# Performance work log

Measured on AMD Instinct MI355X. Metric: run time of the kernel, lower is better.

## Reference

```python
import jax, jax.numpy as jnp
import numpy as np

N_NODES = 100000
N_EDGES = 1280000
D_IN = 64
D_HID = 64
D_OUT = 1
N_GRAPHS = 512


def setup_inputs() -> dict:
    key = jax.random.key(0)
    ks = jax.random.split(key, 12)
    x = jax.random.normal(ks[0], (N_NODES, D_IN), dtype=jnp.float32)
    edge_index = jax.random.randint(ks[1], (2, N_EDGES), 0, N_NODES, dtype=jnp.int32)
    batch = jnp.sort(jax.random.randint(ks[2], (N_NODES,), 0, N_GRAPHS, dtype=jnp.int32))
    s = 0.1
    w0 = jax.random.normal(ks[3], (D_IN, D_HID), dtype=jnp.float32) * s
    b0 = jnp.zeros((D_HID,), dtype=jnp.float32)
    w1 = jax.random.normal(ks[4], (D_HID, D_HID), dtype=jnp.float32) * s
    b1 = jnp.zeros((D_HID,), dtype=jnp.float32)
    w2 = jax.random.normal(ks[5], (D_HID, D_HID), dtype=jnp.float32) * s
    b2 = jnp.zeros((D_HID,), dtype=jnp.float32)
    fc_w = jax.random.normal(ks[6], (D_HID, D_OUT), dtype=jnp.float32) * s
    fc_b = jnp.zeros((D_OUT,), dtype=jnp.float32)
    return {"x": x, "edge_index": edge_index, "batch": batch,
            "w0": w0, "b0": b0, "w1": w1, "b1": b1, "w2": w2, "b2": b2,
            "fc_w": fc_w, "fc_b": fc_b}


def _gcn_conv(x, w, b, src, dst):
    # PyG GCNConv: h = x @ W; out_i = sum_j norm_ij * h_j over (A + I), sym norm.
    h = x @ w                                           # [N, H]
    ones = jnp.ones((src.shape[0],), dtype=h.dtype)
    deg = jax.ops.segment_sum(ones, dst, num_segments=N_NODES) + 1.0  # +1 self-loop
    dinv = jax.lax.rsqrt(deg)                           # [N]
    norm = dinv[src] * dinv[dst]                        # [E]
    agg = jax.ops.segment_sum(h[src] * norm[:, None], dst, num_segments=N_NODES)
    agg = agg + h * (dinv * dinv)[:, None]              # self-loop term
    return agg + b


def reference(x, edge_index, batch, w0, b0, w1, b1, w2, b2, fc_w, fc_b):
    src, dst = edge_index[0], edge_index[1]
    # 3 stacked GCNConv + relu (dropout is identity in eval mode)
    h = jax.nn.relu(_gcn_conv(x, w0, b0, src, dst))
    h = jax.nn.relu(_gcn_conv(h, w1, b1, src, dst))
    h = jax.nn.relu(_gcn_conv(h, w2, b2, src, dst))
    # global mean pool per graph
    sums = jax.ops.segment_sum(h, batch, num_segments=N_GRAPHS)        # [G, H]
    cnt = jax.ops.segment_sum(jnp.ones((N_NODES,), h.dtype), batch, num_segments=N_GRAPHS)
    mean = sums / jnp.maximum(cnt, 1.0)[:, None]
    return mean @ fc_w + fc_b                            # [G, 1]
```

## Files before the change

kernel.cpp:

```cpp
#include <hip/hip_runtime.h>
#include <hip/hip_fp16.h>
#include <type_traits>

#define N_NODES 100000
#define N_EDGES 1280000
#define N_GRAPHS 512
#define NBK 196
#define CHUNK 3200
#define NCH 400
#define CAP 8192
#define CAPH 4096
#define GEMM_BLOCKS 391

typedef _Float16 v8h __attribute__((ext_vector_type(8)));
typedef float v4f __attribute__((ext_vector_type(4)));

__device__ inline void fmix_lo(float& acc, unsigned h2, float n) {
    asm volatile("v_fma_mix_f32 %0, %1, %2, %0 op_sel:[0,0,0] op_sel_hi:[1,0,0]"
                 : "+v"(acc) : "v"(h2), "v"(n));
}
__device__ inline void fmix_hi(float& acc, unsigned h2, float n) {
    asm volatile("v_fma_mix_f32 %0, %1, %2, %0 op_sel:[1,0,0] op_sel_hi:[1,0,0]"
                 : "+v"(acc) : "v"(h2), "v"(n));
}


template <typename T, bool FOLD>
__device__ inline void gemm_body(int bid, const T* __restrict__ X,
                                 const float* __restrict__ W,
                                 const float* __restrict__ dinv,
                                 __half* __restrict__ H,
                                 _Float16 (*Wt)[72]) {
    int t = threadIdx.x;
    #pragma unroll
    for (int q = 0; q < 4; q++) {
        int idx = t + q * 256;
        int k = idx >> 4;
        int n0 = (idx & 15) * 4;
        float4 v = ((const float4*)W)[idx];
        Wt[n0 + 0][k] = (_Float16)v.x;
        Wt[n0 + 1][k] = (_Float16)v.y;
        Wt[n0 + 2][k] = (_Float16)v.z;
        Wt[n0 + 3][k] = (_Float16)v.w;
    }
    __syncthreads();

    int wv = t >> 6, lane = t & 63;
    int m = lane & 15, quad = lane >> 4;

    v8h bf[4][2];
    #pragma unroll
    for (int c = 0; c < 4; c++)
        #pragma unroll
        for (int h = 0; h < 2; h++)
            bf[c][h] = *(const v8h*)&Wt[c * 16 + m][h * 32 + quad * 8];

    int base = bid * 256 + wv * 64;
    #pragma unroll
    for (int tt = 0; tt < 4; tt++) {
        int tile = base + tt * 16;
        int rA = min(tile + m, N_NODES - 1);
        v8h a0, a1;
        if constexpr (std::is_same<T, float>::value) {
            const float* xp = (const float*)X + (size_t)rA * 64 + quad * 8;
            float4 p0 = *(const float4*)xp;
            float4 p1 = *(const float4*)(xp + 4);
            float4 p2 = *(const float4*)(xp + 32);
            float4 p3 = *(const float4*)(xp + 36);
            a0 = (v8h){(_Float16)p0.x, (_Float16)p0.y, (_Float16)p0.z, (_Float16)p0.w,
                       (_Float16)p1.x, (_Float16)p1.y, (_Float16)p1.z, (_Float16)p1.w};
            a1 = (v8h){(_Float16)p2.x, (_Float16)p2.y, (_Float16)p2.z, (_Float16)p2.w,
                       (_Float16)p3.x, (_Float16)p3.y, (_Float16)p3.z, (_Float16)p3.w};
        } else {
            const _Float16* xp = (const _Float16*)X + (size_t)rA * 64 + quad * 8;
            a0 = *(const v8h*)xp;
            a1 = *(const v8h*)(xp + 32);
        }
        v4f acc[4];
        #pragma unroll
        for (int c = 0; c < 4; c++) {
            acc[c] = (v4f){0.f, 0.f, 0.f, 0.f};
            acc[c] = __builtin_amdgcn_mfma_f32_16x16x32_f16(a0, bf[c][0], acc[c], 0, 0, 0);
            acc[c] = __builtin_amdgcn_mfma_f32_16x16x32_f16(a1, bf[c][1], acc[c], 0, 0, 0);
        }
        #pragma unroll
        for (int r = 0; r < 4; r++) {
            int row = tile + quad * 4 + r;
            if (row < N_NODES) {
                float dv = FOLD ? dinv[row] : 1.0f;
                __half* hp = H + (size_t)row * 64 + m;
                #pragma unroll
                for (int c = 0; c < 4; c++)
                    hp[c * 16] = __float2half(FOLD ? acc[c][r] * dv : acc[c][r]);
            }
        }
    }
}

template <typename T, bool FOLD>
__global__ __launch_bounds__(256) void gemm_mfma(const T* __restrict__ X,
                                                 const float* __restrict__ W,
                                                 const float* __restrict__ dinv,
                                                 __half* __restrict__ H) {
    __shared__ _Float16 Wt[64][72];
    gemm_body<T, FOLD>(blockIdx.x, X, W, dinv, H, Wt);
}


#define SC_BUF   0
#define SC_LCNT  (CHUNK * 8)
#define SC_LLOC  (SC_LCNT + NBK * 4)
#define SC_LCUR  (SC_LLOC + NBK * 4)
#define SC_S     (SC_LCUR + NBK * 4)
#define SC_BYTES (SC_S + 256 * 4)

__global__ __launch_bounds__(256) void scatter_gemm(const int* __restrict__ src,
                                                    const int* __restrict__ dst,
                                                    int* __restrict__ bcur,
                                                    int2* __restrict__ pairs,
                                                    const float* __restrict__ x,
                                                    const float* __restrict__ w0,
                                                    __half* __restrict__ H) {
    alignas(16) __shared__ char smem[SC_BYTES];
    if (blockIdx.x >= NCH) {
        gemm_body<float, false>(blockIdx.x - NCH, x, w0, nullptr, H,
                                (_Float16(*)[72])smem);
        return;
    }
    int2* buf  = (int2*)(smem + SC_BUF);
    int*  lcnt = (int*)(smem + SC_LCNT);
    int*  lloc = (int*)(smem + SC_LLOC);
    int*  lcur = (int*)(smem + SC_LCUR);
    int*  s    = (int*)(smem + SC_S);
    int t = threadIdx.x;
    for (int k = t; k < NBK; k += 256) { lcnt[k] = 0; lcur[k] = 0; }
    __syncthreads();
    int e0 = blockIdx.x * CHUNK;
    for (int i = t; i < CHUNK; i += 256) atomicAdd(&lcnt[dst[e0 + i] >> 9], 1);
    __syncthreads();
    {
        int v = (t < NBK) ? lcnt[t] : 0;
        s[t] = v; __syncthreads();
        for (int d = 1; d < 256; d <<= 1) {
            int xx = (t >= d) ? s[t - d] : 0;
            __syncthreads();
            s[t] += xx;
            __syncthreads();
        }
        if (t < NBK) lloc[t] = s[t] - v;
    }
    __syncthreads();
    for (int i = t; i < CHUNK; i += 256) {
        int d = dst[e0 + i];
        int k = d >> 9;
        int li = lloc[k] + atomicAdd(&lcur[k], 1);
        buf[li] = make_int2(src[e0 + i], d);
    }
    __syncthreads();
    for (int k = t; k < NBK; k += 256) {
        int c = lcnt[k];
        if (c) {
            int g = atomicAdd(&bcur[k * 16], c);
            int lo = lloc[k];
            int2* dstp = pairs + (size_t)k * CAP;
            for (int j = 0; j < c; j++)
                if (g + j < CAP) dstp[g + j] = buf[lo + j];
        }
    }
}


__global__ __launch_bounds__(256) void bucket_place(const int2* __restrict__ pairs,
                                                    const int* __restrict__ bcur,
                                                    int* __restrict__ offs,
                                                    float* __restrict__ dinv,
                                                    int* __restrict__ csr) {
    __shared__ int lcnt[256], lofs[256], lcur[256], red[256];
    __shared__ int lsrc[CAPH];
    int t = threadIdx.x;
    int bb = blockIdx.x;
    int b = bb >> 1, half = bb & 1;
    int node0 = (b << 9) + (half << 8);
    int nn = min(256, N_NODES - node0);
    red[t] = (t < b) ? min(bcur[t * 16], CAP) : 0;
    __syncthreads();
    for (int d = 128; d > 0; d >>= 1) {
        if (t < d) red[t] += red[t + d];
        __syncthreads();
    }
    int bbase = red[0];
    int cnt = min(bcur[b * 16], CAP);
    __syncthreads();
    lcnt[t] = 0; lcur[t] = 0;
    __syncthreads();
    const int2* prs = pairs + (size_t)b * CAP;
    for (int i = t; i < cnt; i += 256) {
        int n = prs[i].y - (b << 9);
        if ((n >> 8) == half) atomicAdd(&lcnt[n & 255], 1);
    }
    __syncthreads();
    int deg = lcnt[t];
    red[t] = deg; __syncthreads();
    for (int d = 1; d < 256; d <<= 1) {
        int xx = (t >= d) ? red[t - d] : 0;
        __syncthreads();
        red[t] += xx;
        __syncthreads();
    }
    lofs[t] = red[t] - deg;
    int total = red[255];
    int beg = bbase + (half ? (cnt - total) : 0);
    if (t < nn) {
        offs[node0 + t] = beg + lofs[t];
        dinv[node0 + t] = 1.0f / sqrtf((float)deg + 1.0f);
    }
    __syncthreads();
    for (int i = t; i < cnt; i += 256) {
        int2 pr = prs[i];
        int n = pr.y - (b << 9);
        if ((n >> 8) == half) {
            int li = lofs[n & 255] + atomicAdd(&lcur[n & 255], 1);
            if (li < CAPH) lsrc[li] = pr.x;
        }
    }
    __syncthreads();
    for (int j = t; j < total; j += 256) csr[beg + j] = lsrc[j];
    if (bb == 0 && t == 0) offs[N_NODES] = N_EDGES;
}


template <bool FULL>
__device__ inline void agg_body(const uint2* __restrict__ Hh, int wid, int lane,
                                const int* __restrict__ offs,
                                const int* __restrict__ csr,
                                const float* __restrict__ dinv,
                                float4& out) {
    int eg = lane >> 4;
    int fq = lane & 15;
    int beg = offs[wid], end = offs[wid + 1];
    float di = dinv[wid];
    uint2 us = Hh[wid * 16 + fq];

    float4 a0 = {0.f, 0.f, 0.f, 0.f};
    float4 a1 = {0.f, 0.f, 0.f, 0.f};
    for (int base = beg; base < end; base += 16) {
        int i0 = base + eg;
        int r0 = csr[i0], r1 = csr[i0 + 4], r2 = csr[i0 + 8], r3 = csr[i0 + 12];
        bool p0 = i0      < end, p1 = i0 + 4  < end,
             p2 = i0 + 8  < end, p3 = i0 + 12 < end;
        int s0 = p0 ? r0 : 0, s1 = p1 ? r1 : 0,
            s2 = p2 ? r2 : 0, s3 = p3 ? r3 : 0;
        uint2 u0 = Hh[(s0 << 4) + fq];
        uint2 u1 = Hh[(s1 << 4) + fq];
        uint2 u2 = Hh[(s2 << 4) + fq];
        uint2 u3 = Hh[(s3 << 4) + fq];
        float n0, n1, n2, n3;
        if constexpr (FULL) {
            float d0 = dinv[s0], d1 = dinv[s1], d2 = dinv[s2], d3 = dinv[s3];
            n0 = p0 ? d0 * di : 0.f;
            n1 = p1 ? d1 * di : 0.f;
            n2 = p2 ? d2 * di : 0.f;
            n3 = p3 ? d3 * di : 0.f;
        } else {
            n0 = p0 ? di : 0.f;
            n1 = p1 ? di : 0.f;
            n2 = p2 ? di : 0.f;
            n3 = p3 ? di : 0.f;
        }
        fmix_lo(a0.x, u0.x, n0); fmix_hi(a0.y, u0.x, n0);
        fmix_lo(a0.z, u0.y, n0); fmix_hi(a0.w, u0.y, n0);
        fmix_lo(a1.x, u1.x, n1); fmix_hi(a1.y, u1.x, n1);
        fmix_lo(a1.z, u1.y, n1); fmix_hi(a1.w, u1.y, n1);
        fmix_lo(a0.x, u2.x, n2); fmix_hi(a0.y, u2.x, n2);
        fmix_lo(a0.z, u2.y, n2); fmix_hi(a0.w, u2.y, n2);
        fmix_lo(a1.x, u3.x, n3); fmix_hi(a1.y, u3.x, n3);
        fmix_lo(a1.z, u3.y, n3); fmix_hi(a1.w, u3.y, n3);
    }
    a0.x += a1.x; a0.y += a1.y; a0.z += a1.z; a0.w += a1.w;
    a0.x += __shfl_xor(a0.x, 16); a0.y += __shfl_xor(a0.y, 16);
    a0.z += __shfl_xor(a0.z, 16); a0.w += __shfl_xor(a0.w, 16);
    a0.x += __shfl_xor(a0.x, 32); a0.y += __shfl_xor(a0.y, 32);
    a0.z += __shfl_xor(a0.z, 32); a0.w += __shfl_xor(a0.w, 32);
    float2 s01 = __half22float2(*(__half2*)&us.x);
    float2 s23 = __half22float2(*(__half2*)&us.y);
    float sw = FULL ? di * di : di;
    out.x = a0.x + s01.x * sw; out.y = a0.y + s01.y * sw;
    out.z = a0.z + s23.x * sw; out.w = a0.w + s23.y * sw;
}

template <bool FULL>
__global__ __launch_bounds__(256) void agg_gcn(const __half* __restrict__ H,
                                               const int* __restrict__ offs,
                                               const int* __restrict__ csr,
                                               const float* __restrict__ dinv,
                                               const float* __restrict__ bias,
                                               __half* __restrict__ Out) {
    int wid = (blockIdx.x * 256 + threadIdx.x) >> 6;
    int lane = threadIdx.x & 63;
    if (wid >= N_NODES) return;
    float4 r;
    agg_body<FULL>((const uint2*)H, wid, lane, offs, csr, dinv, r);
    int fq = lane & 15;
    if ((lane >> 4) == 0) {
        float4 b4 = ((const float4*)bias)[fq];
        __half2 h01 = __float22half2_rn(make_float2(fmaxf(r.x + b4.x, 0.f),
                                                    fmaxf(r.y + b4.y, 0.f)));
        __half2 h23 = __float22half2_rn(make_float2(fmaxf(r.z + b4.z, 0.f),
                                                    fmaxf(r.w + b4.w, 0.f)));
        uint2 u;
        u.x = *(unsigned int*)&h01;
        u.y = *(unsigned int*)&h23;
        ((uint2*)Out)[(size_t)wid * 16 + fq] = u;
    }
}

__global__ __launch_bounds__(256) void agg_gcn_pool(const __half* __restrict__ H,
                                                    const int* __restrict__ offs,
                                                    const int* __restrict__ csr,
                                                    const float* __restrict__ dinv,
                                                    const float* __restrict__ bias,
                                                    const float* __restrict__ fcw,
                                                    float* __restrict__ p) {
    int wid = (blockIdx.x * 256 + threadIdx.x) >> 6;
    int lane = threadIdx.x & 63;
    if (wid >= N_NODES) return;
    float4 r;
    agg_body<false>((const uint2*)H, wid, lane, offs, csr, dinv, r);
    int fq = lane & 15;
    float4 b4 = ((const float4*)bias)[fq];
    float4 f4 = ((const float4*)fcw)[fq];
    float v = fmaxf(r.x + b4.x, 0.f) * f4.x + fmaxf(r.y + b4.y, 0.f) * f4.y
            + fmaxf(r.z + b4.z, 0.f) * f4.z + fmaxf(r.w + b4.w, 0.f) * f4.w;
    v += __shfl_xor(v, 1); v += __shfl_xor(v, 2);
    v += __shfl_xor(v, 4); v += __shfl_xor(v, 8);
    if (lane == 0) p[wid] = v;
}


__device__ inline int lower_bound_batch(const int* __restrict__ batch, int key) {
    int lo = 0, hi = N_NODES;
    while (lo < hi) {
        int mid = (lo + hi) >> 1;
        if (batch[mid] < key) lo = mid + 1; else hi = mid;
    }
    return lo;
}

__global__ __launch_bounds__(256) void graph_reduce(const float* __restrict__ p,
                                                    const int* __restrict__ batch,
                                                    const float* __restrict__ fcb,
                                                    float* __restrict__ out) {
    __shared__ float red[4];
    int g = blockIdx.x;
    int s0 = lower_bound_batch(batch, g);
    int s1 = lower_bound_batch(batch, g + 1);
    float acc = 0.f;
    for (int i = s0 + threadIdx.x; i < s1; i += 256) acc += p[i];
    #pragma unroll
    for (int o = 32; o > 0; o >>= 1) acc += __shfl_xor(acc, o);
    int lane = threadIdx.x & 63, wv = threadIdx.x >> 6;
    if (lane == 0) red[wv] = acc;
    __syncthreads();
    if (threadIdx.x == 0) {
        float sum = red[0] + red[1] + red[2] + red[3];
        out[g] = sum / fmaxf((float)(s1 - s0), 1.f) + fcb[0];
    }
}


extern "C" void kernel_launch(void* const* d_in, const int* in_sizes, int n_in,
                              void* d_out, int out_size, void* d_ws, size_t ws_size,
                              hipStream_t stream) {
    const float* x    = (const float*)d_in[0];
    const int*   ei   = (const int*)d_in[1];
    const int*   batch= (const int*)d_in[2];
    const float* w0   = (const float*)d_in[3];
    const float* b0   = (const float*)d_in[4];
    const float* w1   = (const float*)d_in[5];
    const float* b1   = (const float*)d_in[6];
    const float* w2   = (const float*)d_in[7];
    const float* b2   = (const float*)d_in[8];
    const float* fcw  = (const float*)d_in[9];
    const float* fcb  = (const float*)d_in[10];
    float* out = (float*)d_out;

    const int* src_e = ei;
    const int* dst_e = ei + N_EDGES;

    char* w = (char*)d_ws;
    size_t o = 0;
    int*    bcur  = (int*)(w + o);    o += 256 * 16 * 4;
    int*    offs  = (int*)(w + o);    o += (size_t)(N_NODES + 8) * 4;
    float*  dinv  = (float*)(w + o);  o += (size_t)N_NODES * 4;
    int2*   pairs = (int2*)(w + o);   o += (size_t)NBK * CAP * 8;
    int*    csr   = (int*)(w + o);    o += (size_t)(N_EDGES + 16) * 4;
    __half* bufA  = (__half*)(w + o); o += (size_t)N_NODES * 64 * 2;
    __half* bufB  = (__half*)(w + o); o += (size_t)N_NODES * 64 * 2;
    float*  pvec  = (float*)(w + o);  o += (size_t)N_NODES * 4;

    hipMemsetAsync(bcur, 0, 256 * 16 * 4, stream);

    const int AGG_BLOCKS = (N_NODES + 3) / 4;

    scatter_gemm<<<NCH + GEMM_BLOCKS, 256, 0, stream>>>(src_e, dst_e, bcur, pairs,
                                                        x, w0, bufA);
    bucket_place<<<2 * NBK, 256, 0, stream>>>(pairs, bcur, offs, dinv, csr);

    agg_gcn<true><<<AGG_BLOCKS, 256, 0, stream>>>(bufA, offs, csr, dinv, b0, bufB);

    gemm_mfma<__half, true><<<GEMM_BLOCKS, 256, 0, stream>>>(bufB, w1, dinv, bufA);
    agg_gcn<false><<<AGG_BLOCKS, 256, 0, stream>>>(bufA, offs, csr, dinv, b1, bufB);

    gemm_mfma<__half, true><<<GEMM_BLOCKS, 256, 0, stream>>>(bufB, w2, dinv, bufA);
    agg_gcn_pool<<<AGG_BLOCKS, 256, 0, stream>>>(bufA, offs, csr, dinv, b2, fcw, pvec);

    graph_reduce<<<N_GRAPHS, 256, 0, stream>>>(pvec, batch, fcb, out);
}
```

Measured before the change: 292.3 us.

## Fuse next-layer GEMM into aggregation kernel epilogue with pre-transposed weights

Each aggregation block now computes four nodes' aggregated rows, stages them in shared memory, and immediately multiplies by the next layer's weight matrix via MFMA, folding in dinv. This removes two standalone GEMM launches and one round-trip of the N×64 half activation buffer through global memory. A small prep kernel converts and transposes w1/w2 to fp16 once and also zeroes the bucket counters, replacing the memset. The trade is a block-wide barrier in the aggregation kernel and a 16x16 MFMA tile that only uses 4 of its rows, plus per-block weight reads from global memory.

```diff
diff --git a/kernel.cpp b/kernel.cpp
--- a/kernel.cpp
+++ b/kernel.cpp
@@ -25,12 +25,29 @@
 }
 
 
-template <typename T, bool FOLD>
-__device__ inline void gemm_body(int bid, const T* __restrict__ X,
-                                 const float* __restrict__ W,
-                                 const float* __restrict__ dinv,
-                                 __half* __restrict__ H,
-                                 _Float16 (*Wt)[72]) {
+__global__ __launch_bounds__(256) void wprep(const float* __restrict__ w1,
+                                             const float* __restrict__ w2,
+                                             _Float16* __restrict__ wt1,
+                                             _Float16* __restrict__ wt2,
+                                             int* __restrict__ bcur) {
+    int t = threadIdx.x;
+    const float* W = blockIdx.x ? w2 : w1;
+    _Float16*    O = blockIdx.x ? wt2 : wt1;
+    #pragma unroll
+    for (int q = 0; q < 16; q++) {
+        int idx = t + q * 256;
+        int k = idx >> 6, n = idx & 63;
+        O[n * 64 + k] = (_Float16)W[idx];
+    }
+    for (int i = t + blockIdx.x * 2048; i < (blockIdx.x + 1) * 2048; i += 256)
+        bcur[i] = 0;
+}
+
+
+__device__ inline void gemm_body_f32(int bid, const float* __restrict__ X,
+                                     const float* __restrict__ W,
+                                     __half* __restrict__ H,
+                                     _Float16 (*Wt)[72]) {
     int t = threadIdx.x;
     #pragma unroll
     for (int q = 0; q < 4; q++) {
@@ -60,22 +77,15 @@
     for (int tt = 0; tt < 4; tt++) {
         int tile = base + tt * 16;
         int rA = min(tile + m, N_NODES - 1);
-        v8h a0, a1;
-        if constexpr (std::is_same<T, float>::value) {
-            const float* xp = (const float*)X + (size_t)rA * 64 + quad * 8;
-            float4 p0 = *(const float4*)xp;
-            float4 p1 = *(const float4*)(xp + 4);
-            float4 p2 = *(const float4*)(xp + 32);
-            float4 p3 = *(const float4*)(xp + 36);
-            a0 = (v8h){(_Float16)p0.x, (_Float16)p0.y, (_Float16)p0.z, (_Float16)p0.w,
+        const float* xp = X + (size_t)rA * 64 + quad * 8;
+        float4 p0 = *(const float4*)xp;
+        float4 p1 = *(const float4*)(xp + 4);
+        float4 p2 = *(const float4*)(xp + 32);
+        float4 p3 = *(const float4*)(xp + 36);
+        v8h a0 = (v8h){(_Float16)p0.x, (_Float16)p0.y, (_Float16)p0.z, (_Float16)p0.w,
                        (_Float16)p1.x, (_Float16)p1.y, (_Float16)p1.z, (_Float16)p1.w};
-            a1 = (v8h){(_Float16)p2.x, (_Float16)p2.y, (_Float16)p2.z, (_Float16)p2.w,
+        v8h a1 = (v8h){(_Float16)p2.x, (_Float16)p2.y, (_Float16)p2.z, (_Float16)p2.w,
                        (_Float16)p3.x, (_Float16)p3.y, (_Float16)p3.z, (_Float16)p3.w};
-        } else {
-            const _Float16* xp = (const _Float16*)X + (size_t)rA * 64 + quad * 8;
-            a0 = *(const v8h*)xp;
-            a1 = *(const v8h*)(xp + 32);
-        }
         v4f acc[4];
         #pragma unroll
         for (int c = 0; c < 4; c++) {
@@ -87,23 +97,13 @@
         for (int r = 0; r < 4; r++) {
             int row = tile + quad * 4 + r;
             if (row < N_NODES) {
-                float dv = FOLD ? dinv[row] : 1.0f;
                 __half* hp = H + (size_t)row * 64 + m;
                 #pragma unroll
                 for (int c = 0; c < 4; c++)
-                    hp[c * 16] = __float2half(FOLD ? acc[c][r] * dv : acc[c][r]);
+                    hp[c * 16] = __float2half(acc[c][r]);
             }
         }
     }
-}
-
-template <typename T, bool FOLD>
-__global__ __launch_bounds__(256) void gemm_mfma(const T* __restrict__ X,
-                                                 const float* __restrict__ W,
-                                                 const float* __restrict__ dinv,
-                                                 __half* __restrict__ H) {
-    __shared__ _Float16 Wt[64][72];
-    gemm_body<T, FOLD>(blockIdx.x, X, W, dinv, H, Wt);
 }
 
 
@@ -123,8 +123,7 @@
                                                     __half* __restrict__ H) {
     alignas(16) __shared__ char smem[SC_BYTES];
     if (blockIdx.x >= NCH) {
-        gemm_body<float, false>(blockIdx.x - NCH, x, w0, nullptr, H,
-                                (_Float16(*)[72])smem);
+        gemm_body_f32(blockIdx.x - NCH, x, w0, H, (_Float16(*)[72])smem);
         return;
     }
     int2* buf  = (int2*)(smem + SC_BUF);
@@ -288,20 +287,22 @@
     out.z = a0.z + s23.x * sw; out.w = a0.w + s23.y * sw;
 }
 
+
 template <bool FULL>
-__global__ __launch_bounds__(256) void agg_gcn(const __half* __restrict__ H,
-                                               const int* __restrict__ offs,
-                                               const int* __restrict__ csr,
-                                               const float* __restrict__ dinv,
-                                               const float* __restrict__ bias,
-                                               __half* __restrict__ Out) {
-    int wid = (blockIdx.x * 256 + threadIdx.x) >> 6;
-    int lane = threadIdx.x & 63;
-    if (wid >= N_NODES) return;
+__global__ __launch_bounds__(256) void agg_gemm(const __half* __restrict__ H,
+                                                const int* __restrict__ offs,
+                                                const int* __restrict__ csr,
+                                                const float* __restrict__ dinv,
+                                                const float* __restrict__ bias,
+                                                const _Float16* __restrict__ WT,
+                                                __half* __restrict__ O) {
+    __shared__ _Float16 Xt[4][72];
+    int wv = threadIdx.x >> 6, lane = threadIdx.x & 63;
+    int wid = blockIdx.x * 4 + wv;
     float4 r;
     agg_body<FULL>((const uint2*)H, wid, lane, offs, csr, dinv, r);
-    int fq = lane & 15;
-    if ((lane >> 4) == 0) {
+    int fq = lane & 15, quad = lane >> 4;
+    if (quad == 0) {
         float4 b4 = ((const float4*)bias)[fq];
         __half2 h01 = __float22half2_rn(make_float2(fmaxf(r.x + b4.x, 0.f),
                                                     fmaxf(r.y + b4.y, 0.f)));
@@ -310,9 +311,27 @@
         uint2 u;
         u.x = *(unsigned int*)&h01;
         u.y = *(unsigned int*)&h23;
-        ((uint2*)Out)[(size_t)wid * 16 + fq] = u;
-    }
-}
+        *(uint2*)&Xt[wv][fq * 4] = u;
+    }
+    __syncthreads();
+    v8h a0 = *(const v8h*)&Xt[fq & 3][quad * 8];
+    v8h a1 = *(const v8h*)&Xt[fq & 3][32 + quad * 8];
+    int n = wv * 16 + fq;
+    v8h b0 = *(const v8h*)&WT[n * 64 + quad * 8];
+    v8h b1 = *(const v8h*)&WT[n * 64 + 32 + quad * 8];
+    v4f acc = (v4f){0.f, 0.f, 0.f, 0.f};
+    acc = __builtin_amdgcn_mfma_f32_16x16x32_f16(a0, b0, acc, 0, 0, 0);
+    acc = __builtin_amdgcn_mfma_f32_16x16x32_f16(a1, b1, acc, 0, 0, 0);
+    if (quad == 0) {
+        #pragma unroll
+        for (int rr = 0; rr < 4; rr++) {
+            int row = blockIdx.x * 4 + rr;
+            float dv = dinv[row];
+            O[(size_t)row * 64 + n] = __float2half(acc[rr] * dv);
+        }
+    }
+}
+
 
 __global__ __launch_bounds__(256) void agg_gcn_pool(const __half* __restrict__ H,
                                                     const int* __restrict__ offs,
@@ -389,29 +408,26 @@
 
     char* w = (char*)d_ws;
     size_t o = 0;
-    int*    bcur  = (int*)(w + o);    o += 256 * 16 * 4;
-    int*    offs  = (int*)(w + o);    o += (size_t)(N_NODES + 8) * 4;
-    float*  dinv  = (float*)(w + o);  o += (size_t)N_NODES * 4;
-    int2*   pairs = (int2*)(w + o);   o += (size_t)NBK * CAP * 8;
-    int*    csr   = (int*)(w + o);    o += (size_t)(N_EDGES + 16) * 4;
-    __half* bufA  = (__half*)(w + o); o += (size_t)N_NODES * 64 * 2;
-    __half* bufB  = (__half*)(w + o); o += (size_t)N_NODES * 64 * 2;
-    float*  pvec  = (float*)(w + o);  o += (size_t)N_NODES * 4;
-
-    hipMemsetAsync(bcur, 0, 256 * 16 * 4, stream);
-
-    const int AGG_BLOCKS = (N_NODES + 3) / 4;
-
+    int*      bcur = (int*)(w + o);      o += 256 * 16 * 4;
+    int*      offs = (int*)(w + o);      o += (size_t)(N_NODES + 8) * 4;
+    float*    dinv = (float*)(w + o);    o += (size_t)N_NODES * 4;
+    _Float16* wt1  = (_Float16*)(w + o); o += 64 * 64 * 2;
+    _Float16* wt2  = (_Float16*)(w + o); o += 64 * 64 * 2;
+    int2*     pairs= (int2*)(w + o);     o += (size_t)NBK * CAP * 8;
+    int*      csr  = (int*)(w + o);      o += (size_t)(N_EDGES + 16) * 4;
+    __half*   bufA = (__half*)(w + o);   o += (size_t)N_NODES * 64 * 2;
+    __half*   bufB = (__half*)(w + o);   o += (size_t)N_NODES * 64 * 2;
+    float*    pvec = (float*)(w + o);    o += (size_t)N_NODES * 4;
+
+    const int AGG_BLOCKS = N_NODES / 4;
+
+    wprep<<<2, 256, 0, stream>>>(w1, w2, wt1, wt2, bcur);
     scatter_gemm<<<NCH + GEMM_BLOCKS, 256, 0, stream>>>(src_e, dst_e, bcur, pairs,
                                                         x, w0, bufA);
     bucket_place<<<2 * NBK, 256, 0, stream>>>(pairs, bcur, offs, dinv, csr);
 
-    agg_gcn<true><<<AGG_BLOCKS, 256, 0, stream>>>(bufA, offs, csr, dinv, b0, bufB);
-
-    gemm_mfma<__half, true><<<GEMM_BLOCKS, 256, 0, stream>>>(bufB, w1, dinv, bufA);
-    agg_gcn<false><<<AGG_BLOCKS, 256, 0, stream>>>(bufA, offs, csr, dinv, b1, bufB);
-
-    gemm_mfma<__half, true><<<GEMM_BLOCKS, 256, 0, stream>>>(bufB, w2, dinv, bufA);
+    agg_gemm<true><<<AGG_BLOCKS, 256, 0, stream>>>(bufA, offs, csr, dinv, b0, wt1, bufB);
+    agg_gemm<false><<<AGG_BLOCKS, 256, 0, stream>>>(bufB, offs, csr, dinv, b1, wt2, bufA);
     agg_gcn_pool<<<AGG_BLOCKS, 256, 0, stream>>>(bufA, offs, csr, dinv, b2, fcw, pvec);
 
     graph_reduce<<<N_GRAPHS, 256, 0, stream>>>(pvec, batch, fcb, out);
```

New measurement: 299.7 us. +2.5%, slower.
